# Performance work log

Hardware: AMD Instinct MI355X
Metric: run time of the kernel (lower is better)

The kernel has to match this reference:

```python
import jax, jax.numpy as jnp
import numpy as np

MARGIN1 = 0.5
ALPHA = 1.0
GAMMA = 1.0
THETA = 0.1
K = 8  # num_instances per identity

N = 4096
D_FEA = 512
N_CLS = 751
D_SIDE = 1024


def setup_inputs() -> dict:
    key = jax.random.key(0)
    ks = jax.random.split(key, 5)
    return {
        "cls_fea": jax.random.normal(ks[0], (N, N_CLS), dtype=jnp.float32),
        "l2_side": jax.random.normal(ks[1], (N, D_SIDE), dtype=jnp.float32),
        "l3_side": jax.random.normal(ks[2], (N, D_SIDE), dtype=jnp.float32),
        "l4_side": jax.random.normal(ks[3], (N, D_SIDE), dtype=jnp.float32),
        "input_fea": jax.random.normal(ks[4], (N, D_FEA), dtype=jnp.float32),
        # PK sampling: exactly K consecutive samples per identity
        "targets": jnp.arange(N, dtype=jnp.int32) // K,
    }


def _rank_terms(dist, mask, n):
    """Vectorized replacement of the per-row rank-mining python loop."""
    j = jnp.arange(n)
    k = jnp.arange(K)

    def row(drow, mrow):
        order = jnp.argsort(drow)          # ascending distances
        sd = drow[order]                   # sort_dist
        pm = mrow[order]                   # positive mask in rank order
        # negatives that sneaked into the top-K ranks (== full_index leftovers)
        flag_neg = (~pm) & (j < K)
        # positives ranked outside top-K (== wrong_indice)
        flag_pos = pm & (j >= K)
        m = jnp.sum(flag_neg)              # left_wrong_num (counts match by construction)
        # wrong negatives in ascending rank order, padded to K slots
        neg_ord = jnp.argsort(jnp.where(flag_neg, j, j + n))[:K]
        # wrong positives in DESCENDING rank order (loop iterates reverse-sorted)
        pos_ord = jnp.argsort(jnp.where(flag_pos, -j, 1))[:K]
        wneg = sd[neg_ord]
        wpos = sd[pos_ord]
        valid = k < m
        most_wrong_neg = wneg[0]           # smallest wrong-negative distance
        ratio = (most_wrong_neg - wneg) / (most_wrong_neg + 1e-12)
        weight = (m - k).astype(sd.dtype) * jnp.exp(ratio)
        loss = jnp.sum(jnp.where(valid, weight * (wpos - wneg) + MARGIN1, 0.0))
        return loss, (m == 0)

    return jax.vmap(row)(dist, mask)


def reference(cls_fea, l2_side, l3_side, l4_side, input_fea, targets):
    n = input_fea.shape[0]
    # pairwise euclidean distance, clamped like torch .clamp(min=1e-12).sqrt()
    sq = jnp.sum(input_fea * input_fea, axis=1)
    d2 = sq[:, None] + sq[None, :] - 2.0 * (input_fea @ input_fea.T)
    dist = jnp.sqrt(jnp.maximum(d2, 1e-12))
    mask = targets[:, None] == targets[None, :]

    losses, corrects = _rank_terms(dist, mask, n)
    rank_loss = jnp.sum(losses) / n
    prec = jnp.mean(corrects.astype(jnp.float32))

    # cross entropy
    logp = jax.nn.log_softmax(cls_fea, axis=-1)
    xent = -jnp.mean(jnp.take_along_axis(logp, targets[:, None].astype(jnp.int32), axis=1))

    # side losses: frobenius norms of differences
    side_loss = jnp.sqrt(jnp.sum((l4_side - l2_side) ** 2)) + \
                jnp.sqrt(jnp.sum((l4_side - l3_side) ** 2))

    total = ALPHA * rank_loss + GAMMA * xent + THETA * side_loss

    # accuracy() helper (undefined in source): standard top-1 on input_fea vs targets
    acc = jnp.mean((jnp.argmax(input_fea, axis=1).astype(targets.dtype) == targets).astype(jnp.float32))
    prec2 = jnp.maximum(prec, acc)
    return total, prec2
```

## Files before the change

### kernel.cpp

```cpp
#include <hip/hip_runtime.h>
#include <hip/hip_bf16.h>
#include <math.h>

#define NROWS 4096
#define DFEA  512
#define NCLS  751
#define DSIDE 1024

typedef __attribute__((ext_vector_type(8))) short short8;
typedef __attribute__((ext_vector_type(4))) float f32x4;

__device__ __forceinline__ float wave_sum(float v) {
#pragma unroll
  for (int off = 32; off > 0; off >>= 1) v += __shfl_xor(v, off, 64);
  return v;
}

__device__ __forceinline__ void load_lds16(const void* g, void* l) {
  __builtin_amdgcn_global_load_lds((const __attribute__((address_space(1))) void*)g,
                                   (__attribute__((address_space(3))) void*)l, 16, 0, 0);
}

__device__ __forceinline__ void ins8(float t8[8], float x) {
#pragma unroll
  for (int q = 0; q < 8; ++q) {
    const float lo = fminf(t8[q], x);
    x = fmaxf(t8[q], x);
    t8[q] = lo;
  }
}

#define CE(x, i, j) { const float ce_lo = fminf(x[i], x[j]); x[j] = fmaxf(x[i], x[j]); x[i] = ce_lo; }

__device__ __forceinline__ void merge_sorted8(float a[8], int mask) {
  float b[8];
#pragma unroll
  for (int i = 0; i < 8; ++i) b[i] = __shfl_xor(a[i], mask, 64);
  float c[8];
#pragma unroll
  for (int i = 0; i < 8; ++i) c[i] = fminf(a[i], b[7 - i]);
  CE(c, 0, 4) CE(c, 1, 5) CE(c, 2, 6) CE(c, 3, 7)
  CE(c, 0, 2) CE(c, 1, 3) CE(c, 4, 6) CE(c, 5, 7)
  CE(c, 0, 1) CE(c, 2, 3) CE(c, 4, 5) CE(c, 6, 7)
#pragma unroll
  for (int i = 0; i < 8; ++i) a[i] = c[i];
}

__device__ __forceinline__ unsigned short bf16bits(float v) {
  union { __hip_bfloat16 b; unsigned short u; } cv;
  cv.b = __float2bfloat16(v);
  return cv.u;
}

__global__ __launch_bounds__(256) void k_row_sq_acc(const float* __restrict__ fea,
                                                    const int* __restrict__ tgt,
                                                    float* __restrict__ sq,
                                                    float* __restrict__ pa) {
  const int lane = threadIdx.x & 63;
  const int wid  = threadIdx.x >> 6;
  const int row  = blockIdx.x * 4 + wid;
  const float* x = fea + (size_t)row * DFEA;
  float s = 0.0f, bv = -1e30f;
  int bi = 0;
#pragma unroll
  for (int q = 0; q < DFEA / 64; ++q) {
    const int c = lane + q * 64;
    const float v = x[c];
    s += v * v;
    if (v > bv) { bv = v; bi = c; }
  }
#pragma unroll
  for (int off = 32; off > 0; off >>= 1) {
    s += __shfl_xor(s, off, 64);
    const float ov = __shfl_xor(bv, off, 64);
    const int   oi = __shfl_xor(bi, off, 64);
    if (ov > bv || (ov == bv && oi < bi)) { bv = ov; bi = oi; }
  }
  __shared__ float red[4];
  if (lane == 0) {
    sq[row]  = s;
    red[wid] = (bi == tgt[row]) ? 1.0f : 0.0f;
  }
  __syncthreads();
  if (threadIdx.x == 0) pa[blockIdx.x] = red[0] + red[1] + red[2] + red[3];
}

__global__ __launch_bounds__(256) void k_split(const float* __restrict__ fea,
                                               unsigned short* __restrict__ Fhi,
                                               unsigned short* __restrict__ Flo) {
  const int i = blockIdx.x * 256 + threadIdx.x;
  const float4 x = ((const float4*)fea)[i];
  ushort4 h, l;
  float hf;
  h.x = bf16bits(x.x); hf = __bfloat162float(__ushort_as_bfloat16(h.x)); l.x = bf16bits(x.x - hf);
  h.y = bf16bits(x.y); hf = __bfloat162float(__ushort_as_bfloat16(h.y)); l.y = bf16bits(x.y - hf);
  h.z = bf16bits(x.z); hf = __bfloat162float(__ushort_as_bfloat16(h.z)); l.z = bf16bits(x.z - hf);
  h.w = bf16bits(x.w); hf = __bfloat162float(__ushort_as_bfloat16(h.w)); l.w = bf16bits(x.w - hf);
  ((ushort4*)Fhi)[i] = h;
  ((ushort4*)Flo)[i] = l;
}

__global__ __launch_bounds__(256) void k_gemm_mfma(const unsigned short* __restrict__ Fhi,
                                                   const unsigned short* __restrict__ Flo,
                                                   const float* __restrict__ sq,
                                                   float* __restrict__ posw,
                                                   float* __restrict__ part) {
  const int bx = blockIdx.x, by = blockIdx.y;
  const int R0 = by * 128, C0 = bx * 128;
  const int tid = threadIdx.x;
  const int lane = tid & 63, wid = tid >> 6;
  const int wr = wid >> 1, wc = wid & 1;
  const int l15 = lane & 15, l4 = lane >> 4;

  __shared__ __attribute__((aligned(16))) char smem[33280];
  const __hip_bfloat16 (*As)[64] = (const __hip_bfloat16(*)[64])smem;
  const __hip_bfloat16 (*Bs)[64] = (const __hip_bfloat16(*)[64])(smem + 16384);
  float (*dtile)[130] = (float(*)[130])smem;

  f32x4 acc[4][4];
#pragma unroll
  for (int m = 0; m < 4; ++m)
#pragma unroll
    for (int n = 0; n < 4; ++n) acc[m][n] = (f32x4){0.0f, 0.0f, 0.0f, 0.0f};

  for (int kt = 0; kt < 24; ++kt) {
    const unsigned short* Aseg = (kt < 16) ? Fhi : Flo;
    const unsigned short* Bseg = (kt >= 8 && kt < 16) ? Flo : Fhi;
    const int ks = (kt & 7) * 64;
    __syncthreads();
#pragma unroll
    for (int i = 0; i < 4; ++i) {
      const int flat = i * 256 + tid;
      const int row = flat >> 3, c8 = flat & 7;
      load_lds16(Aseg + (size_t)(R0 + row) * DFEA + ks + c8 * 8,
                 smem + (i * 256 + wid * 64) * 16);
      load_lds16(Bseg + (size_t)(C0 + row) * DFEA + ks + c8 * 8,
                 smem + 16384 + (i * 256 + wid * 64) * 16);
    }
    __syncthreads();
#pragma unroll
    for (int kk = 0; kk < 2; ++kk) {
      short8 af[4], bf[4];
#pragma unroll
      for (int m = 0; m < 4; ++m)
        af[m] = *(const short8*)&As[wr * 64 + m * 16 + l15][kk * 32 + l4 * 8];
#pragma unroll
      for (int n = 0; n < 4; ++n)
        bf[n] = *(const short8*)&Bs[wc * 64 + n * 16 + l15][kk * 32 + l4 * 8];
#pragma unroll
      for (int m = 0; m < 4; ++m)
#pragma unroll
        for (int n = 0; n < 4; ++n)
          acc[m][n] = __builtin_amdgcn_mfma_f32_16x16x32_bf16(af[m], bf[n], acc[m][n], 0, 0, 0);
    }
  }

  float sqi[4][4], sqj[4];
#pragma unroll
  for (int m = 0; m < 4; ++m)
#pragma unroll
    for (int r = 0; r < 4; ++r) sqi[m][r] = sq[R0 + wr * 64 + m * 16 + l4 * 4 + r];
#pragma unroll
  for (int n = 0; n < 4; ++n) sqj[n] = sq[C0 + wc * 64 + n * 16 + l15];

  const bool diag = (bx == by);

  for (int h = 0; h < 2; ++h) {
    __syncthreads();
    if (wr == h) {
#pragma unroll
      for (int m = 0; m < 4; ++m)
#pragma unroll
        for (int n = 0; n < 4; ++n)
#pragma unroll
          for (int r = 0; r < 4; ++r)
            dtile[m * 16 + l4 * 4 + r][wc * 64 + n * 16 + l15] =
                sqi[m][r] + sqj[n] - 2.0f * acc[m][n][r];
    }
    __syncthreads();
    const int r = tid >> 2, q = tid & 3;
    const int rg = R0 + h * 64 + r;
    float t8[8];
#pragma unroll
    for (int i = 0; i < 8; ++i) t8[i] = 1e30f;
    if (diag) {
      for (int s = 0; s < 32; ++s) {
        const int cg = C0 + q * 32 + s;
        const float v = dtile[r][q * 32 + s];
        if (((rg ^ cg) >> 3) == 0) posw[(size_t)rg * 8 + (cg & 7)] = v;
        else ins8(t8, v);
      }
    } else {
      for (int s = 0; s < 32; ++s) ins8(t8, dtile[r][q * 32 + s]);
    }
    merge_sorted8(t8, 1);
    merge_sorted8(t8, 2);
    if (q == 0) {
      const float4 o0 = {t8[0], t8[1], t8[2], t8[3]};
      const float4 o1 = {t8[4], t8[5], t8[6], t8[7]};
      *(float4*)&part[(size_t)rg * 256 + bx * 8] = o0;
      *(float4*)&part[(size_t)rg * 256 + bx * 8 + 4] = o1;
    }
  }
}

__global__ __launch_bounds__(256) void k_final2(const float* __restrict__ part,
                                                const float* __restrict__ posw,
                                                float* __restrict__ pl,
                                                float* __restrict__ pc) {
  const int lane = threadIdx.x & 63, w = threadIdx.x >> 6;
  const int row = blockIdx.x * 4 + w;
  float a[8];
  if (lane < 32) {
    const float4 v0 = *(const float4*)&part[(size_t)row * 256 + lane * 8];
    const float4 v1 = *(const float4*)&part[(size_t)row * 256 + lane * 8 + 4];
    a[0] = v0.x; a[1] = v0.y; a[2] = v0.z; a[3] = v0.w;
    a[4] = v1.x; a[5] = v1.y; a[6] = v1.z; a[7] = v1.w;
  } else {
#pragma unroll
    for (int i = 0; i < 8; ++i) a[i] = 1e30f;
  }
  merge_sorted8(a, 1);
  merge_sorted8(a, 2);
  merge_sorted8(a, 4);
  merge_sorted8(a, 8);
  merge_sorted8(a, 16);
  __shared__ float red[8];
  if (lane == 0) {
    float nd[8];
#pragma unroll
    for (int i = 0; i < 8; ++i) nd[i] = sqrtf(fmaxf(a[i], 1e-12f));
    float s8[8];
#pragma unroll
    for (int i = 0; i < 8; ++i) s8[i] = 1e30f;
#pragma unroll
    for (int i = 0; i < 8; ++i)
      ins8(s8, sqrtf(fmaxf(posw[(size_t)row * 8 + i], 1e-12f)));
    int ip = 0, in_ = 0;
#pragma unroll
    for (int s = 0; s < 8; ++s) {
      const bool takeNeg = (in_ < 8) && (ip >= 8 || nd[in_] < s8[ip]);
      if (takeNeg) ++in_; else ++ip;
    }
    const int m = in_;
    float loss = 0.0f;
    const float n0 = nd[0];
    for (int k = 0; k < m; ++k)
      loss += (float)(m - k) * expf((n0 - nd[k]) / (n0 + 1e-12f)) * (s8[7 - k] - nd[k]) + 0.5f;
    red[w] = loss;
    red[4 + w] = (m == 0) ? 1.0f : 0.0f;
  }
  __syncthreads();
  if (threadIdx.x == 0) {
    pl[blockIdx.x] = red[0] + red[1] + red[2] + red[3];
    pc[blockIdx.x] = red[4] + red[5] + red[6] + red[7];
  }
}

__global__ __launch_bounds__(256) void k_xent(const float* __restrict__ cls,
                                              const int* __restrict__ tgt,
                                              float* __restrict__ px) {
  const int lane = threadIdx.x & 63, wid = threadIdx.x >> 6;
  const int row = blockIdx.x * 4 + wid;
  const float* x = cls + (size_t)row * NCLS;
  float mx = -1e30f;
  for (int c = lane; c < NCLS; c += 64) mx = fmaxf(mx, x[c]);
#pragma unroll
  for (int off = 32; off > 0; off >>= 1) mx = fmaxf(mx, __shfl_xor(mx, off, 64));
  float se = 0.0f;
  for (int c = lane; c < NCLS; c += 64) se += expf(x[c] - mx);
  se = wave_sum(se);
  __shared__ float red[4];
  if (lane == 0) red[wid] = logf(se) + mx - x[tgt[row]];
  __syncthreads();
  if (threadIdx.x == 0) px[blockIdx.x] = red[0] + red[1] + red[2] + red[3];
}

__global__ __launch_bounds__(256) void k_side(const float* __restrict__ l2,
                                              const float* __restrict__ l3,
                                              const float* __restrict__ l4,
                                              float* __restrict__ ps2,
                                              float* __restrict__ ps3) {
  const int nt = gridDim.x * blockDim.x;
  float s2 = 0.0f, s3 = 0.0f;
  for (int i = blockIdx.x * blockDim.x + threadIdx.x; i < (NROWS * DSIDE / 4); i += nt) {
    const float4 a2 = ((const float4*)l2)[i];
    const float4 a3 = ((const float4*)l3)[i];
    const float4 a4 = ((const float4*)l4)[i];
    float dx = a4.x - a2.x, dy = a4.y - a2.y, dz = a4.z - a2.z, dw = a4.w - a2.w;
    s2 += dx * dx + dy * dy + dz * dz + dw * dw;
    dx = a4.x - a3.x; dy = a4.y - a3.y; dz = a4.z - a3.z; dw = a4.w - a3.w;
    s3 += dx * dx + dy * dy + dz * dz + dw * dw;
  }
  s2 = wave_sum(s2);
  s3 = wave_sum(s3);
  __shared__ float red[8];
  const int wid = threadIdx.x >> 6, lane = threadIdx.x & 63;
  if (lane == 0) { red[wid] = s2; red[4 + wid] = s3; }
  __syncthreads();
  if (threadIdx.x == 0) {
    ps2[blockIdx.x] = red[0] + red[1] + red[2] + red[3];
    ps3[blockIdx.x] = red[4] + red[5] + red[6] + red[7];
  }
}

__global__ __launch_bounds__(256) void k_finalize(const float* __restrict__ pl,
                                                  const float* __restrict__ pc,
                                                  const float* __restrict__ px,
                                                  const float* __restrict__ pa,
                                                  const float* __restrict__ ps2,
                                                  const float* __restrict__ ps3,
                                                  float* __restrict__ out) {
  const int t = threadIdx.x;
  float s[6] = {0, 0, 0, 0, 0, 0};
  for (int i = t; i < 1024; i += 256) {
    s[0] += pl[i]; s[1] += pc[i]; s[2] += px[i];
    s[3] += pa[i]; s[4] += ps2[i]; s[5] += ps3[i];
  }
  __shared__ float red[6][4];
  const int lane = t & 63, w = t >> 6;
#pragma unroll
  for (int j = 0; j < 6; ++j) {
    s[j] = wave_sum(s[j]);
    if (lane == 0) red[j][w] = s[j];
  }
  __syncthreads();
  if (t == 0) {
    const float rank_loss = (red[0][0] + red[0][1] + red[0][2] + red[0][3]) / (float)NROWS;
    const float prec      = (red[1][0] + red[1][1] + red[1][2] + red[1][3]) / (float)NROWS;
    const float xent      = (red[2][0] + red[2][1] + red[2][2] + red[2][3]) / (float)NROWS;
    const float acc       = (red[3][0] + red[3][1] + red[3][2] + red[3][3]) / (float)NROWS;
    const float side      = sqrtf(red[4][0] + red[4][1] + red[4][2] + red[4][3]) +
                            sqrtf(red[5][0] + red[5][1] + red[5][2] + red[5][3]);
    out[0] = rank_loss + xent + 0.1f * side;
    out[1] = fmaxf(prec, acc);
  }
}

extern "C" void kernel_launch(void* const* d_in, const int* in_sizes, int n_in,
                              void* d_out, int out_size, void* d_ws, size_t ws_size,
                              hipStream_t stream) {
  (void)in_sizes; (void)n_in; (void)out_size; (void)ws_size;
  const float* cls = (const float*)d_in[0];
  const float* l2  = (const float*)d_in[1];
  const float* l3  = (const float*)d_in[2];
  const float* l4  = (const float*)d_in[3];
  const float* fea = (const float*)d_in[4];
  const int*   tgt = (const int*)d_in[5];
  float* out = (float*)d_out;

  float* sq   = (float*)d_ws;
  unsigned short* Fhi = (unsigned short*)(sq + NROWS);
  unsigned short* Flo = Fhi + (size_t)NROWS * DFEA;
  float* part = (float*)(Flo + (size_t)NROWS * DFEA);
  float* posw = part + (size_t)NROWS * 256;
  float* pl   = posw + (size_t)NROWS * 8;
  float* pc   = pl + 1024;
  float* px   = pc + 1024;
  float* pa   = px + 1024;
  float* ps2  = pa + 1024;
  float* ps3  = ps2 + 1024;

  k_row_sq_acc<<<dim3(NROWS / 4), dim3(256), 0, stream>>>(fea, tgt, sq, pa);
  k_split<<<dim3(NROWS * DFEA / 4 / 256), dim3(256), 0, stream>>>(fea, Fhi, Flo);
  k_gemm_mfma<<<dim3(32, 32), dim3(256), 0, stream>>>(Fhi, Flo, sq, posw, part);
  k_final2<<<dim3(NROWS / 4), dim3(256), 0, stream>>>(part, posw, pl, pc);
  k_xent<<<dim3(NROWS / 4), dim3(256), 0, stream>>>(cls, tgt, px);
  k_side<<<dim3(1024), dim3(256), 0, stream>>>(l2, l3, l4, ps2, ps3);
  k_finalize<<<dim3(1), dim3(256), 0, stream>>>(pl, pc, px, pa, ps2, ps3, out);
}
```

Baseline: 221.1 us.

## Exploit distance symmetry in GEMM and fuse prep and misc kernels

The distance GEMM now computes only the upper-triangle blocks. Off-diagonal blocks also extract column-wise top-8 and write them into the transposed row's partial slot, which roughly halves MFMA work. The row-norm/argmax and bf16 hi/lo split kernels are merged into one pass over the features, and the cross-entropy and side-loss kernels are merged into one launch. LDS column access in the row scan is rotated to reduce bank conflicts. The trade-offs are an added column-scan pass over LDS in off-diagonal blocks and half the blocks exiting early, which leaves the triangular grid load-imbalanced.

```diff
diff --git a/kernel.cpp b/kernel.cpp
--- a/kernel.cpp
+++ b/kernel.cpp
@@ -52,22 +52,38 @@
   return cv.u;
 }
 
-__global__ __launch_bounds__(256) void k_row_sq_acc(const float* __restrict__ fea,
-                                                    const int* __restrict__ tgt,
-                                                    float* __restrict__ sq,
-                                                    float* __restrict__ pa) {
+__global__ __launch_bounds__(256) void k_prep(const float* __restrict__ fea,
+                                              const int* __restrict__ tgt,
+                                              float* __restrict__ sq,
+                                              float* __restrict__ pa,
+                                              unsigned short* __restrict__ Fhi,
+                                              unsigned short* __restrict__ Flo) {
   const int lane = threadIdx.x & 63;
   const int wid  = threadIdx.x >> 6;
   const int row  = blockIdx.x * 4 + wid;
-  const float* x = fea + (size_t)row * DFEA;
+  const float4* xr = (const float4*)(fea + (size_t)row * DFEA);
+  ushort4* hr = (ushort4*)(Fhi + (size_t)row * DFEA);
+  ushort4* lr = (ushort4*)(Flo + (size_t)row * DFEA);
   float s = 0.0f, bv = -1e30f;
   int bi = 0;
 #pragma unroll
-  for (int q = 0; q < DFEA / 64; ++q) {
-    const int c = lane + q * 64;
-    const float v = x[c];
-    s += v * v;
-    if (v > bv) { bv = v; bi = c; }
+  for (int q = 0; q < 2; ++q) {
+    const int i4 = q * 64 + lane;
+    const float4 v = xr[i4];
+    s += v.x * v.x + v.y * v.y + v.z * v.z + v.w * v.w;
+    const int c0 = i4 * 4;
+    if (v.x > bv) { bv = v.x; bi = c0; }
+    if (v.y > bv) { bv = v.y; bi = c0 + 1; }
+    if (v.z > bv) { bv = v.z; bi = c0 + 2; }
+    if (v.w > bv) { bv = v.w; bi = c0 + 3; }
+    ushort4 h, l;
+    float hf;
+    h.x = bf16bits(v.x); hf = __bfloat162float(__ushort_as_bfloat16(h.x)); l.x = bf16bits(v.x - hf);
+    h.y = bf16bits(v.y); hf = __bfloat162float(__ushort_as_bfloat16(h.y)); l.y = bf16bits(v.y - hf);
+    h.z = bf16bits(v.z); hf = __bfloat162float(__ushort_as_bfloat16(h.z)); l.z = bf16bits(v.z - hf);
+    h.w = bf16bits(v.w); hf = __bfloat162float(__ushort_as_bfloat16(h.w)); l.w = bf16bits(v.w - hf);
+    hr[i4] = h;
+    lr[i4] = l;
   }
 #pragma unroll
   for (int off = 32; off > 0; off >>= 1) {
@@ -83,21 +99,6 @@
   }
   __syncthreads();
   if (threadIdx.x == 0) pa[blockIdx.x] = red[0] + red[1] + red[2] + red[3];
-}
-
-__global__ __launch_bounds__(256) void k_split(const float* __restrict__ fea,
-                                               unsigned short* __restrict__ Fhi,
-                                               unsigned short* __restrict__ Flo) {
-  const int i = blockIdx.x * 256 + threadIdx.x;
-  const float4 x = ((const float4*)fea)[i];
-  ushort4 h, l;
-  float hf;
-  h.x = bf16bits(x.x); hf = __bfloat162float(__ushort_as_bfloat16(h.x)); l.x = bf16bits(x.x - hf);
-  h.y = bf16bits(x.y); hf = __bfloat162float(__ushort_as_bfloat16(h.y)); l.y = bf16bits(x.y - hf);
-  h.z = bf16bits(x.z); hf = __bfloat162float(__ushort_as_bfloat16(h.z)); l.z = bf16bits(x.z - hf);
-  h.w = bf16bits(x.w); hf = __bfloat162float(__ushort_as_bfloat16(h.w)); l.w = bf16bits(x.w - hf);
-  ((ushort4*)Fhi)[i] = h;
-  ((ushort4*)Flo)[i] = l;
 }
 
 __global__ __launch_bounds__(256) void k_gemm_mfma(const unsigned short* __restrict__ Fhi,
@@ -106,6 +107,7 @@
                                                    float* __restrict__ posw,
                                                    float* __restrict__ part) {
   const int bx = blockIdx.x, by = blockIdx.y;
+  if (bx < by) return;
   const int R0 = by * 128, C0 = bx * 128;
   const int tid = threadIdx.x;
   const int lane = tid & 63, wid = tid >> 6;
@@ -165,6 +167,10 @@
 
   const bool diag = (bx == by);
 
+  float c8a[8];
+#pragma unroll
+  for (int i = 0; i < 8; ++i) c8a[i] = 1e30f;
+
   for (int h = 0; h < 2; ++h) {
     __syncthreads();
     if (wr == h) {
@@ -178,28 +184,47 @@
                 sqi[m][r] + sqj[n] - 2.0f * acc[m][n][r];
     }
     __syncthreads();
-    const int r = tid >> 2, q = tid & 3;
-    const int rg = R0 + h * 64 + r;
-    float t8[8];
-#pragma unroll
-    for (int i = 0; i < 8; ++i) t8[i] = 1e30f;
-    if (diag) {
-      for (int s = 0; s < 32; ++s) {
-        const int cg = C0 + q * 32 + s;
-        const float v = dtile[r][q * 32 + s];
-        if (((rg ^ cg) >> 3) == 0) posw[(size_t)rg * 8 + (cg & 7)] = v;
-        else ins8(t8, v);
+    {
+      const int r = tid >> 2, q = tid & 3;
+      const int rg = R0 + h * 64 + r;
+      float t8[8];
+#pragma unroll
+      for (int i = 0; i < 8; ++i) t8[i] = 1e30f;
+      if (diag) {
+        for (int s = 0; s < 32; ++s) {
+          const int cl = q * 32 + ((s + 9 * q) & 31);
+          const int cg = C0 + cl;
+          const float v = dtile[r][cl];
+          if (((rg ^ cg) >> 3) == 0) posw[(size_t)rg * 8 + (cg & 7)] = v;
+          else ins8(t8, v);
+        }
+      } else {
+        for (int s = 0; s < 32; ++s) ins8(t8, dtile[r][q * 32 + ((s + 9 * q) & 31)]);
       }
-    } else {
-      for (int s = 0; s < 32; ++s) ins8(t8, dtile[r][q * 32 + s]);
-    }
-    merge_sorted8(t8, 1);
-    merge_sorted8(t8, 2);
-    if (q == 0) {
-      const float4 o0 = {t8[0], t8[1], t8[2], t8[3]};
-      const float4 o1 = {t8[4], t8[5], t8[6], t8[7]};
-      *(float4*)&part[(size_t)rg * 256 + bx * 8] = o0;
-      *(float4*)&part[(size_t)rg * 256 + bx * 8 + 4] = o1;
+      merge_sorted8(t8, 1);
+      merge_sorted8(t8, 2);
+      if (q == 0) {
+        const float4 o0 = {t8[0], t8[1], t8[2], t8[3]};
+        const float4 o1 = {t8[4], t8[5], t8[6], t8[7]};
+        *(float4*)&part[(size_t)rg * 256 + bx * 8] = o0;
+        *(float4*)&part[(size_t)rg * 256 + bx * 8 + 4] = o1;
+      }
+    }
+    if (!diag) {
+      const int c = tid >> 1, q2 = tid & 1;
+      for (int s = 0; s < 32; ++s) ins8(c8a, dtile[q2 * 32 + s][c]);
+    }
+  }
+
+  if (!diag) {
+    const int c = tid >> 1, q2 = tid & 1;
+    merge_sorted8(c8a, 1);
+    if (q2 == 0) {
+      const int cg = C0 + c;
+      const float4 o0 = {c8a[0], c8a[1], c8a[2], c8a[3]};
+      const float4 o1 = {c8a[4], c8a[5], c8a[6], c8a[7]};
+      *(float4*)&part[(size_t)cg * 256 + by * 8] = o0;
+      *(float4*)&part[(size_t)cg * 256 + by * 8 + 4] = o1;
     }
   }
 }
@@ -257,50 +282,51 @@
   }
 }
 
-__global__ __launch_bounds__(256) void k_xent(const float* __restrict__ cls,
+__global__ __launch_bounds__(256) void k_misc(const float* __restrict__ cls,
                                               const int* __restrict__ tgt,
-                                              float* __restrict__ px) {
-  const int lane = threadIdx.x & 63, wid = threadIdx.x >> 6;
-  const int row = blockIdx.x * 4 + wid;
-  const float* x = cls + (size_t)row * NCLS;
-  float mx = -1e30f;
-  for (int c = lane; c < NCLS; c += 64) mx = fmaxf(mx, x[c]);
-#pragma unroll
-  for (int off = 32; off > 0; off >>= 1) mx = fmaxf(mx, __shfl_xor(mx, off, 64));
-  float se = 0.0f;
-  for (int c = lane; c < NCLS; c += 64) se += expf(x[c] - mx);
-  se = wave_sum(se);
-  __shared__ float red[4];
-  if (lane == 0) red[wid] = logf(se) + mx - x[tgt[row]];
-  __syncthreads();
-  if (threadIdx.x == 0) px[blockIdx.x] = red[0] + red[1] + red[2] + red[3];
-}
-
-__global__ __launch_bounds__(256) void k_side(const float* __restrict__ l2,
+                                              const float* __restrict__ l2,
                                               const float* __restrict__ l3,
                                               const float* __restrict__ l4,
+                                              float* __restrict__ px,
                                               float* __restrict__ ps2,
                                               float* __restrict__ ps3) {
-  const int nt = gridDim.x * blockDim.x;
-  float s2 = 0.0f, s3 = 0.0f;
-  for (int i = blockIdx.x * blockDim.x + threadIdx.x; i < (NROWS * DSIDE / 4); i += nt) {
-    const float4 a2 = ((const float4*)l2)[i];
-    const float4 a3 = ((const float4*)l3)[i];
-    const float4 a4 = ((const float4*)l4)[i];
-    float dx = a4.x - a2.x, dy = a4.y - a2.y, dz = a4.z - a2.z, dw = a4.w - a2.w;
-    s2 += dx * dx + dy * dy + dz * dz + dw * dw;
-    dx = a4.x - a3.x; dy = a4.y - a3.y; dz = a4.z - a3.z; dw = a4.w - a3.w;
-    s3 += dx * dx + dy * dy + dz * dz + dw * dw;
-  }
-  s2 = wave_sum(s2);
-  s3 = wave_sum(s3);
-  __shared__ float red[8];
-  const int wid = threadIdx.x >> 6, lane = threadIdx.x & 63;
-  if (lane == 0) { red[wid] = s2; red[4 + wid] = s3; }
-  __syncthreads();
-  if (threadIdx.x == 0) {
-    ps2[blockIdx.x] = red[0] + red[1] + red[2] + red[3];
-    ps3[blockIdx.x] = red[4] + red[5] + red[6] + red[7];
+  const int lane = threadIdx.x & 63, wid = threadIdx.x >> 6;
+  if (blockIdx.x < 1024) {
+    const int row = blockIdx.x * 4 + wid;
+    const float* x = cls + (size_t)row * NCLS;
+    float mx = -1e30f;
+    for (int c = lane; c < NCLS; c += 64) mx = fmaxf(mx, x[c]);
+#pragma unroll
+    for (int off = 32; off > 0; off >>= 1) mx = fmaxf(mx, __shfl_xor(mx, off, 64));
+    float se = 0.0f;
+    for (int c = lane; c < NCLS; c += 64) se += expf(x[c] - mx);
+    se = wave_sum(se);
+    __shared__ float redx[4];
+    if (lane == 0) redx[wid] = logf(se) + mx - x[tgt[row]];
+    __syncthreads();
+    if (threadIdx.x == 0) px[blockIdx.x] = redx[0] + redx[1] + redx[2] + redx[3];
+  } else {
+    const int bid = blockIdx.x - 1024;
+    const int nt = 1024 * 256;
+    float s2 = 0.0f, s3 = 0.0f;
+    for (int i = bid * 256 + threadIdx.x; i < (NROWS * DSIDE / 4); i += nt) {
+      const float4 a2 = ((const float4*)l2)[i];
+      const float4 a3 = ((const float4*)l3)[i];
+      const float4 a4 = ((const float4*)l4)[i];
+      float dx = a4.x - a2.x, dy = a4.y - a2.y, dz = a4.z - a2.z, dw = a4.w - a2.w;
+      s2 += dx * dx + dy * dy + dz * dz + dw * dw;
+      dx = a4.x - a3.x; dy = a4.y - a3.y; dz = a4.z - a3.z; dw = a4.w - a3.w;
+      s3 += dx * dx + dy * dy + dz * dz + dw * dw;
+    }
+    s2 = wave_sum(s2);
+    s3 = wave_sum(s3);
+    __shared__ float red[8];
+    if (lane == 0) { red[wid] = s2; red[4 + wid] = s3; }
+    __syncthreads();
+    if (threadIdx.x == 0) {
+      ps2[bid] = red[0] + red[1] + red[2] + red[3];
+      ps3[bid] = red[4] + red[5] + red[6] + red[7];
+    }
   }
 }
 
@@ -361,11 +387,9 @@
   float* ps2  = pa + 1024;
   float* ps3  = ps2 + 1024;
 
-  k_row_sq_acc<<<dim3(NROWS / 4), dim3(256), 0, stream>>>(fea, tgt, sq, pa);
-  k_split<<<dim3(NROWS * DFEA / 4 / 256), dim3(256), 0, stream>>>(fea, Fhi, Flo);
+  k_prep<<<dim3(NROWS / 4), dim3(256), 0, stream>>>(fea, tgt, sq, pa, Fhi, Flo);
   k_gemm_mfma<<<dim3(32, 32), dim3(256), 0, stream>>>(Fhi, Flo, sq, posw, part);
   k_final2<<<dim3(NROWS / 4), dim3(256), 0, stream>>>(part, posw, pl, pc);
-  k_xent<<<dim3(NROWS / 4), dim3(256), 0, stream>>>(cls, tgt, px);
-  k_side<<<dim3(1024), dim3(256), 0, stream>>>(l2, l3, l4, ps2, ps3);
+  k_misc<<<dim3(2048), dim3(256), 0, stream>>>(cls, tgt, l2, l3, l4, px, ps2, ps3);
   k_finalize<<<dim3(1), dim3(256), 0, stream>>>(pl, pc, px, pa, ps2, ps3, out);
 }
```

Result: slower. 276.5 us (+25.1%).
